# Kernel tuning notes

Measured on AMD Instinct MI355X. Metric: run time of the kernel, lower is better.

The kernel has to match this reference:

```python
import jax, jax.numpy as jnp
import numpy as np

EMBD_SIZE = 128
NUM_HEADS = 8
HEAD_SIZE = 16

def setup_inputs() -> dict:
    key = jax.random.key(0)
    ks = jax.random.split(key, 6)
    B, S = 8, 2048
    x = jax.random.normal(ks[0], (B, S, EMBD_SIZE), dtype=jnp.float32)
    # per-head Linear weights, torch layout [out, in] stacked over heads -> [H, hs, E]
    sc = 1.0 / np.sqrt(EMBD_SIZE)
    Wk = jax.random.normal(ks[1], (NUM_HEADS, HEAD_SIZE, EMBD_SIZE), dtype=jnp.float32) * sc
    Wq = jax.random.normal(ks[2], (NUM_HEADS, HEAD_SIZE, EMBD_SIZE), dtype=jnp.float32) * sc
    Wv = jax.random.normal(ks[3], (NUM_HEADS, HEAD_SIZE, EMBD_SIZE), dtype=jnp.float32) * sc
    Wp = jax.random.normal(ks[4], (EMBD_SIZE, NUM_HEADS * HEAD_SIZE), dtype=jnp.float32) * sc
    bp = jax.random.normal(ks[5], (EMBD_SIZE,), dtype=jnp.float32) * 0.01
    return {"x": x, "Wk": Wk, "Wq": Wq, "Wv": Wv, "Wp": Wp, "bp": bp}

def reference(x, Wk, Wq, Wv, Wp, bp):
    # x: [B,S,E]; W{k,q,v}: [H,hs,E]; Wp: [E,H*hs]
    B, S, E = x.shape
    H, hs, _ = Wk.shape
    q = jnp.einsum('bse,hde->bhsd', x, Wq)
    k = jnp.einsum('bse,hde->bhsd', x, Wk)
    v = jnp.einsum('bse,hde->bhsd', x, Wv)
    # NOTE: original code MULTIPLIES by sqrt(head_size) (k.shape[-1]**0.5)
    scores = jnp.einsum('bhsd,bhtd->bhst', q, k) * (hs ** 0.5)
    wei = jax.nn.softmax(scores, axis=-1)  # dropout is identity in eval mode
    out = jnp.einsum('bhst,bhtd->bhsd', wei, v)
    # concat heads along last dim: [B,S,H*hs]
    out = out.transpose(0, 2, 1, 3).reshape(B, S, H * hs)
    return out @ Wp.T + bp
```

## Files before the change

kernel.cpp:

```cpp
#include <hip/hip_runtime.h>
#include <hip/hip_bf16.h>

constexpr int Bb  = 8;
constexpr int Ss  = 2048;
constexpr int Ee  = 128;
constexpr int Hh  = 8;
constexpr int HSs = 16;
constexpr int QKVSZ = Bb * Hh * Ss * HSs;

typedef _Float16 f16;
typedef __attribute__((ext_vector_type(8)))  _Float16 f16x8;
typedef __attribute__((ext_vector_type(16))) float f32x16;

constexpr float QSCALE = 5.770780163555854f;

__device__ __forceinline__ unsigned pack_rtz(float lo, float hi) {
    union { __fp16 __attribute__((ext_vector_type(2))) h; unsigned u; } c;
    c.h = __builtin_amdgcn_cvt_pkrtz(lo, hi);
    return c.u;
}
__device__ __forceinline__ unsigned pack_rne(float lo, float hi) {
    union { __attribute__((ext_vector_type(2))) _Float16 h; unsigned u; } c;
    c.h[0] = (f16)lo; c.h[1] = (f16)hi;
    return c.u;
}

__global__ __launch_bounds__(256) void prep_kernel(
    const float* __restrict__ Wq, const float* __restrict__ Wk,
    const float* __restrict__ Wv, const float* __restrict__ Wp,
    f16* __restrict__ wh, f16* __restrict__ vo)
{
    const int idx = blockIdx.x * 256 + threadIdx.x;
    if (idx < 16384) {
        const int i = idx * 4;
        const float* src = (i < 16384) ? (Wq + i)
                         : (i < 32768) ? (Wk + i - 16384)
                         : (i < 49152) ? (Wv + i - 32768) : (Wp + i - 49152);
        float4 v = *(const float4*)src;
        union { f16 h[4]; uint2 u; } c;
        c.h[0] = (f16)v.x; c.h[1] = (f16)v.y; c.h[2] = (f16)v.z; c.h[3] = (f16)v.w;
        *(uint2*)(wh + i) = c.u;
    } else {
        const int p = idx - 16384;
        const int lane32 = p & 31, g = (p >> 5) & 3, it = (p >> 7) & 31, bh = p >> 12;
        const int lanep = 16 + (lane32 & 15) + (lane32 >> 4) * 32;
        const unsigned one2 = 0x3C003C00u;
        uint4 val = ((lane32 & 15) == 0) ? (uint4){one2, one2, one2, one2}
                                         : (uint4){0, 0, 0, 0};
        *(uint4*)(vo + (size_t)bh * 65536 + it * 2048 + g * 512 + lanep * 8) = val;
    }
}

__global__ __launch_bounds__(256) void qkv_kernel(
    const float* __restrict__ x, const f16* __restrict__ wh,
    f16* __restrict__ qo, f16* __restrict__ ko, f16* __restrict__ vo)
{
    constexpr int LDW = 136;
    __shared__ __align__(16) f16 Xs[32 * LDW];

    const int rowbase = blockIdx.x * 32;

    for (int idx = threadIdx.x; idx < 32 * 32; idx += 256) {
        const int r = idx >> 5, cp = idx & 31;
        float4 v = *(const float4*)(x + (size_t)(rowbase + r) * Ee + cp * 4);
        union { f16 h[4]; uint2 u; } c;
        c.h[0] = (f16)v.x; c.h[1] = (f16)v.y; c.h[2] = (f16)v.z; c.h[3] = (f16)v.w;
        *(uint2*)&Xs[r * LDW + cp * 4] = c.u;
    }
    __syncthreads();

    const int wv_ = threadIdx.x >> 6, lane = threadIdx.x & 63;
    const int h = lane >> 5, n31 = lane & 31;

    f16x8 A[8];
#pragma unroll
    for (int t = 0; t < 8; ++t)
        A[t] = *(const f16x8*)&Xs[n31 * LDW + 16 * t + 8 * h];
    __syncthreads();

    const int c = wv_ * 32 + n31;
    const int b = rowbase >> 11;
    const int s0 = rowbase & 2047;
    const int head = c >> 4, d = c & 15;
    const int bh = b * Hh + head;

    {
        const f16* wr = wh + 2 * 16384 + (size_t)c * Ee + 8 * h;
        f32x16 acc = {};
#pragma unroll
        for (int t = 0; t < 8; ++t)
            acc = __builtin_amdgcn_mfma_f32_32x32x16_f16(A[t], *(const f16x8*)(wr + 16 * t), acc, 0, 0, 0);
#pragma unroll
        for (int r = 0; r < 16; ++r) {
            const int row = (r & 3) + 8 * (r >> 2) + 4 * h;
            Xs[row * LDW + c] = (f16)acc[r];
        }
    }

#pragma unroll
    for (int mat = 0; mat < 2; ++mat) {
        const f16* wr = wh + mat * 16384 + (size_t)c * Ee + 8 * h;
        f32x16 acc = {};
#pragma unroll
        for (int t = 0; t < 8; ++t)
            acc = __builtin_amdgcn_mfma_f32_32x32x16_f16(A[t], *(const f16x8*)(wr + 16 * t), acc, 0, 0, 0);
        f16* dst = (mat == 0) ? qo : ko;
        const float scale = (mat == 1) ? QSCALE : 1.f;
#pragma unroll
        for (int r = 0; r < 16; ++r) {
            const int s = s0 + (r & 3) + 8 * (r >> 2) + 4 * h;
            dst[((size_t)bh * Ss + s) * HSs + d] = (f16)(acc[r] * scale);
        }
    }
    __syncthreads();

    const int it = s0 >> 6, g0 = (s0 >> 4) & 3;
    for (int p = threadIdx.x; p < 512; p += 256) {
        const int gl = p >> 8, hd = (p >> 5) & 7, dd = (p >> 1) & 15, eh = p & 1;
        union { f16 hv[8]; uint4 u; } pkt;
#pragma unroll
        for (int j = 0; j < 8; ++j)
            pkt.hv[j] = Xs[(gl * 16 + eh * 8 + j) * LDW + hd * 16 + dd];
        *(uint4*)(vo + (size_t)(b * Hh + hd) * 65536 + it * 2048
                  + (g0 + gl) * 512 + (dd + 32 * eh) * 8) = pkt.u;
    }
}

__device__ __forceinline__ void cb_exchange(const unsigned* pw, int h,
                                            f16x8& Blo, f16x8& Bhi) {
    unsigned exa = (unsigned)__shfl_xor((int)(h ? pw[0] : pw[2]), 32, 64);
    unsigned exb = (unsigned)__shfl_xor((int)(h ? pw[1] : pw[3]), 32, 64);
    unsigned exc = (unsigned)__shfl_xor((int)(h ? pw[4] : pw[6]), 32, 64);
    unsigned exd = (unsigned)__shfl_xor((int)(h ? pw[5] : pw[7]), 32, 64);
    union { unsigned u[4]; f16x8 v; } B1, B2;
    if (h == 0) {
        B1.u[0] = pw[0]; B1.u[1] = pw[1]; B1.u[2] = exa; B1.u[3] = exb;
        B2.u[0] = pw[4]; B2.u[1] = pw[5]; B2.u[2] = exc; B2.u[3] = exd;
    } else {
        B1.u[0] = exa; B1.u[1] = exb; B1.u[2] = pw[2]; B1.u[3] = pw[3];
        B2.u[0] = exc; B2.u[1] = exd; B2.u[2] = pw[6]; B2.u[3] = pw[7];
    }
    Blo = B1.v; Bhi = B2.v;
}

__global__ __launch_bounds__(128, 3) void attn_kernel(
    const f16* __restrict__ qg, const f16* __restrict__ kg,
    const f16* __restrict__ vg, f16* __restrict__ og)
{
    __shared__ float cmb[32 * 20];

    const int blk  = blockIdx.x;
    const int bh   = (blk & 7) * 8 + (blk >> 9);
    const int qblk = (blk >> 3) & 63;
    const int wv_  = threadIdx.x >> 6;
    const int lane = threadIdx.x & 63;
    const int h    = lane >> 5;
    const int q31  = lane & 31;
    const int qbase = qblk * 32;

    const f16x8 qf = *(const f16x8*)(qg + ((size_t)bh * Ss + qbase + q31) * HSs + 8 * h);

    const f16* pk = kg + (size_t)bh * Ss * HSs + wv_ * 1024 * HSs + q31 * 16 + 8 * h;
    const f16* pv = vg + (size_t)bh * 65536 + wv_ * 32768 + lane * 8;

    f16x8 ka0 = *(const f16x8*)pk;
    f16x8 ka1 = *(const f16x8*)(pk + 512);
    f16x8 va0 = *(const f16x8*)(pv);
    f16x8 va1 = *(const f16x8*)(pv + 512);
    f16x8 va2 = *(const f16x8*)(pv + 1024);
    f16x8 va3 = *(const f16x8*)(pv + 1536);

    f32x16 acc = {};
    const f32x16 z16 = {};
    float m = -1e30f;

    for (int it = 0; it < 16; ++it) {
        f16x8 nk0, nk1, nv0, nv1, nv2, nv3;
        if (it < 15) {
            pk += 1024; pv += 2048;
            nk0 = *(const f16x8*)pk;
            nk1 = *(const f16x8*)(pk + 512);
            nv0 = *(const f16x8*)(pv);
            nv1 = *(const f16x8*)(pv + 512);
            nv2 = *(const f16x8*)(pv + 1024);
            nv3 = *(const f16x8*)(pv + 1536);
        }

        f32x16 st0 = __builtin_amdgcn_mfma_f32_32x32x16_f16(ka0, qf, z16, 0, 0, 0);
        f32x16 st1 = __builtin_amdgcn_mfma_f32_32x32x16_f16(ka1, qf, z16, 0, 0, 0);

        float t0[8];
#pragma unroll
        for (int t = 0; t < 8; ++t)
            t0[t] = fmaxf(fmaxf(st0[t], st0[t + 8]), fmaxf(st1[t], st1[t + 8]));
#pragma unroll
        for (int t = 0; t < 4; ++t) t0[t] = fmaxf(t0[t], t0[t + 4]);
        float mx = fmaxf(fmaxf(t0[0], t0[1]), fmaxf(t0[2], t0[3]));
        mx = fmaxf(mx, __shfl_xor(mx, 32, 64));
        const float mnew = fmaxf(m, mx);
        const float corr = __builtin_amdgcn_exp2f(m - mnew);
#pragma unroll
        for (int r = 0; r < 9; ++r) acc[r] *= corr;
        m = mnew;

#pragma unroll
        for (int t = 0; t < 16; ++t) st0[t] = __builtin_amdgcn_exp2f(st0[t] - mnew);
#pragma unroll
        for (int t = 0; t < 16; ++t) st1[t] = __builtin_amdgcn_exp2f(st1[t] - mnew);
        unsigned pw0[8], pw1[8];
#pragma unroll
        for (int r = 0; r < 8; ++r) pw0[r] = pack_rtz(st0[2 * r], st0[2 * r + 1]);
#pragma unroll
        for (int r = 0; r < 8; ++r) pw1[r] = pack_rtz(st1[2 * r], st1[2 * r + 1]);
        f16x8 B1, B2, B3, B4;
        cb_exchange(pw0, h, B1, B2);
        cb_exchange(pw1, h, B3, B4);

        acc = __builtin_amdgcn_mfma_f32_32x32x16_f16(va0, B1, acc, 0, 0, 0);
        acc = __builtin_amdgcn_mfma_f32_32x32x16_f16(va1, B2, acc, 0, 0, 0);
        acc = __builtin_amdgcn_mfma_f32_32x32x16_f16(va2, B3, acc, 0, 0, 0);
        acc = __builtin_amdgcn_mfma_f32_32x32x16_f16(va3, B4, acc, 0, 0, 0);

        ka0 = nk0; ka1 = nk1;
        va0 = nv0; va1 = nv1; va2 = nv2; va3 = nv3;
    }

    const float lp = acc[8] + __shfl_xor(acc[8], 32, 64);

    if (wv_ == 1) {
        float* base = &cmb[q31 * 20];
#pragma unroll
        for (int j = 0; j < 4; ++j) { base[4 * h + j] = acc[j]; base[8 + 4 * h + j] = acc[4 + j]; }
        base[16] = lp; base[17] = m;
    }
    __syncthreads();
    if (wv_ == 0) {
        const float* base = &cmb[q31 * 20];
        const float l2 = base[16], m2 = base[17];
        const float M  = fmaxf(m, m2);
        const float c1 = __builtin_amdgcn_exp2f(m - M);
        const float c2 = __builtin_amdgcn_exp2f(m2 - M);
        const float l  = lp * c1 + l2 * c2;
        const float inv = 1.f / l;
        float o[8];
#pragma unroll
        for (int j = 0; j < 4; ++j) {
            o[j]     = (acc[j]     * c1 + base[4 * h + j]     * c2) * inv;
            o[4 + j] = (acc[4 + j] * c1 + base[8 + 4 * h + j] * c2) * inv;
        }
        const int b = bh >> 3, head = bh & 7;
        f16* op = og + ((size_t)b * Ss + qbase + q31) * Ee + head * HSs;
        uint2 lo = { pack_rne(o[0], o[1]), pack_rne(o[2], o[3]) };
        uint2 hi = { pack_rne(o[4], o[5]), pack_rne(o[6], o[7]) };
        *(uint2*)(op + 4 * h)     = lo;
        *(uint2*)(op + 8 + 4 * h) = hi;
    }
}

__global__ __launch_bounds__(256) void proj_kernel(
    const f16* __restrict__ oh, const f16* __restrict__ wph,
    const float* __restrict__ bp, float* __restrict__ out)
{
    constexpr int LDW = 136;
    __shared__ __align__(16) f16 Os[32 * LDW];
    const int rowbase = blockIdx.x * 32;

    for (int idx = threadIdx.x; idx < 512; idx += 256) {
        const int r = idx >> 4, cp = idx & 15;
        *(f16x8*)&Os[r * LDW + cp * 8] =
            *(const f16x8*)(oh + (size_t)(rowbase + r) * Ee + cp * 8);
    }
    __syncthreads();

    const int wv_ = threadIdx.x >> 6, lane = threadIdx.x & 63;
    const int h = lane >> 5, n31 = lane & 31;

    f16x8 A[8];
#pragma unroll
    for (int t = 0; t < 8; ++t)
        A[t] = *(const f16x8*)&Os[n31 * LDW + 16 * t + 8 * h];

    const int e = wv_ * 32 + n31;
    const f16* wr = wph + (size_t)e * Ee + 8 * h;
    f32x16 acc = {};
#pragma unroll
    for (int t = 0; t < 8; ++t)
        acc = __builtin_amdgcn_mfma_f32_32x32x16_f16(A[t], *(const f16x8*)(wr + 16 * t), acc, 0, 0, 0);

    const float bias = bp[e];
#pragma unroll
    for (int r = 0; r < 16; ++r) {
        const int R = rowbase + (r & 3) + 8 * (r >> 2) + 4 * h;
        out[(size_t)R * Ee + e] = acc[r] + bias;
    }
}

extern "C" void kernel_launch(void* const* d_in, const int* in_sizes, int n_in,
                              void* d_out, int out_size, void* d_ws, size_t ws_size,
                              hipStream_t stream)
{
    const float* x  = (const float*)d_in[0];
    const float* Wk = (const float*)d_in[1];
    const float* Wq = (const float*)d_in[2];
    const float* Wv = (const float*)d_in[3];
    const float* Wp = (const float*)d_in[4];
    const float* bp = (const float*)d_in[5];
    float* out = (float*)d_out;

    f16* ws = (f16*)d_ws;
    f16* qh = ws;
    f16* kh = ws + (size_t)QKVSZ;
    f16* vh = ws + (size_t)2 * QKVSZ;
    f16* oh = ws + (size_t)4 * QKVSZ;
    f16* wh = ws + (size_t)5 * QKVSZ;

    prep_kernel<<<1088, 256, 0, stream>>>(Wq, Wk, Wv, Wp, wh, vh);
    qkv_kernel<<<Bb * Ss / 32, 256, 0, stream>>>(x, wh, qh, kh, vh);
    attn_kernel<<<Bb * Hh * (Ss / 32), 128, 0, stream>>>(qh, kh, vh, oh);
    proj_kernel<<<Bb * Ss / 32, 256, 0, stream>>>(oh, wh + 49152, bp, out);
}
```

Before: 142.3 us.

## Fuse output projection into attention kernel, one wave per head

```diff
diff --git a/kernel.cpp b/kernel.cpp
--- a/kernel.cpp
+++ b/kernel.cpp
@@ -143,25 +143,28 @@
     Blo = B1.v; Bhi = B2.v;
 }
 
-__global__ __launch_bounds__(128, 3) void attn_kernel(
+__global__ __launch_bounds__(512, 2) void attn_kernel(
     const f16* __restrict__ qg, const f16* __restrict__ kg,
-    const f16* __restrict__ vg, f16* __restrict__ og)
-{
-    __shared__ float cmb[32 * 20];
+    const f16* __restrict__ vg, const f16* __restrict__ wph,
+    const float* __restrict__ bp, float* __restrict__ out)
+{
+    constexpr int LDW = 136;
+    __shared__ __align__(16) f16 Os[32 * LDW];
 
     const int blk  = blockIdx.x;
-    const int bh   = (blk & 7) * 8 + (blk >> 9);
-    const int qblk = (blk >> 3) & 63;
+    const int b    = blk & 7;
+    const int qblk = blk >> 3;
     const int wv_  = threadIdx.x >> 6;
     const int lane = threadIdx.x & 63;
     const int h    = lane >> 5;
     const int q31  = lane & 31;
     const int qbase = qblk * 32;
+    const int bh   = b * Hh + wv_;
 
     const f16x8 qf = *(const f16x8*)(qg + ((size_t)bh * Ss + qbase + q31) * HSs + 8 * h);
 
-    const f16* pk = kg + (size_t)bh * Ss * HSs + wv_ * 1024 * HSs + q31 * 16 + 8 * h;
-    const f16* pv = vg + (size_t)bh * 65536 + wv_ * 32768 + lane * 8;
+    const f16* pk = kg + (size_t)bh * Ss * HSs + q31 * 16 + 8 * h;
+    const f16* pv = vg + (size_t)bh * 65536 + lane * 8;
 
     f16x8 ka0 = *(const f16x8*)pk;
     f16x8 ka1 = *(const f16x8*)(pk + 512);
@@ -174,9 +177,9 @@
     const f32x16 z16 = {};
     float m = -1e30f;
 
-    for (int it = 0; it < 16; ++it) {
+    for (int it = 0; it < Ss / 64; ++it) {
         f16x8 nk0, nk1, nv0, nv1, nv2, nv3;
-        if (it < 15) {
+        if (it < Ss / 64 - 1) {
             pk += 1024; pv += 2048;
             nk0 = *(const f16x8*)pk;
             nk1 = *(const f16x8*)(pk + 512);
@@ -225,73 +228,38 @@
         va0 = nv0; va1 = nv1; va2 = nv2; va3 = nv3;
     }
 
-    const float lp = acc[8] + __shfl_xor(acc[8], 32, 64);
-
-    if (wv_ == 1) {
-        float* base = &cmb[q31 * 20];
-#pragma unroll
-        for (int j = 0; j < 4; ++j) { base[4 * h + j] = acc[j]; base[8 + 4 * h + j] = acc[4 + j]; }
-        base[16] = lp; base[17] = m;
-    }
-    __syncthreads();
-    if (wv_ == 0) {
-        const float* base = &cmb[q31 * 20];
-        const float l2 = base[16], m2 = base[17];
-        const float M  = fmaxf(m, m2);
-        const float c1 = __builtin_amdgcn_exp2f(m - M);
-        const float c2 = __builtin_amdgcn_exp2f(m2 - M);
-        const float l  = lp * c1 + l2 * c2;
-        const float inv = 1.f / l;
-        float o[8];
-#pragma unroll
-        for (int j = 0; j < 4; ++j) {
-            o[j]     = (acc[j]     * c1 + base[4 * h + j]     * c2) * inv;
-            o[4 + j] = (acc[4 + j] * c1 + base[8 + 4 * h + j] * c2) * inv;
-        }
-        const int b = bh >> 3, head = bh & 7;
-        f16* op = og + ((size_t)b * Ss + qbase + q31) * Ee + head * HSs;
-        uint2 lo = { pack_rne(o[0], o[1]), pack_rne(o[2], o[3]) };
-        uint2 hi = { pack_rne(o[4], o[5]), pack_rne(o[6], o[7]) };
-        *(uint2*)(op + 4 * h)     = lo;
-        *(uint2*)(op + 8 + 4 * h) = hi;
-    }
-}
-
-__global__ __launch_bounds__(256) void proj_kernel(
-    const f16* __restrict__ oh, const f16* __restrict__ wph,
-    const float* __restrict__ bp, float* __restrict__ out)
-{
-    constexpr int LDW = 136;
-    __shared__ __align__(16) f16 Os[32 * LDW];
-    const int rowbase = blockIdx.x * 32;
-
-    for (int idx = threadIdx.x; idx < 512; idx += 256) {
-        const int r = idx >> 4, cp = idx & 15;
-        *(f16x8*)&Os[r * LDW + cp * 8] =
-            *(const f16x8*)(oh + (size_t)(rowbase + r) * Ee + cp * 8);
-    }
-    __syncthreads();
-
-    const int wv_ = threadIdx.x >> 6, lane = threadIdx.x & 63;
-    const int h = lane >> 5, n31 = lane & 31;
-
-    f16x8 A[8];
-#pragma unroll
-    for (int t = 0; t < 8; ++t)
-        A[t] = *(const f16x8*)&Os[n31 * LDW + 16 * t + 8 * h];
-
-    const int e = wv_ * 32 + n31;
-    const f16* wr = wph + (size_t)e * Ee + 8 * h;
-    f32x16 acc = {};
-#pragma unroll
-    for (int t = 0; t < 8; ++t)
-        acc = __builtin_amdgcn_mfma_f32_32x32x16_f16(A[t], *(const f16x8*)(wr + 16 * t), acc, 0, 0, 0);
-
-    const float bias = bp[e];
-#pragma unroll
-    for (int r = 0; r < 16; ++r) {
-        const int R = rowbase + (r & 3) + 8 * (r >> 2) + 4 * h;
-        out[(size_t)R * Ee + e] = acc[r] + bias;
+    const float l = acc[8] + __shfl_xor(acc[8], 32, 64);
+    const float inv = 1.f / l;
+    {
+        unsigned w0 = pack_rne(acc[0] * inv, acc[1] * inv);
+        unsigned w1 = pack_rne(acc[2] * inv, acc[3] * inv);
+        unsigned w2 = pack_rne(acc[4] * inv, acc[5] * inv);
+        unsigned w3 = pack_rne(acc[6] * inv, acc[7] * inv);
+        f16* od = &Os[q31 * LDW + wv_ * HSs];
+        *(uint2*)(od + 4 * h)     = (uint2){w0, w1};
+        *(uint2*)(od + 8 + 4 * h) = (uint2){w2, w3};
+    }
+    __syncthreads();
+
+    if (wv_ < 4) {
+        f16x8 A[8];
+#pragma unroll
+        for (int t = 0; t < 8; ++t)
+            A[t] = *(const f16x8*)&Os[q31 * LDW + 16 * t + 8 * h];
+
+        const int e = wv_ * 32 + q31;
+        const f16* wr = wph + (size_t)e * Ee + 8 * h;
+        f32x16 pacc = {};
+#pragma unroll
+        for (int t = 0; t < 8; ++t)
+            pacc = __builtin_amdgcn_mfma_f32_32x32x16_f16(A[t], *(const f16x8*)(wr + 16 * t), pacc, 0, 0, 0);
+
+        const float bias = bp[e];
+#pragma unroll
+        for (int r = 0; r < 16; ++r) {
+            const int R = qbase + (r & 3) + 8 * (r >> 2) + 4 * h;
+            out[((size_t)b * Ss + R) * Ee + e] = pacc[r] + bias;
+        }
     }
 }
 
@@ -311,11 +279,9 @@
     f16* qh = ws;
     f16* kh = ws + (size_t)QKVSZ;
     f16* vh = ws + (size_t)2 * QKVSZ;
-    f16* oh = ws + (size_t)4 * QKVSZ;
-    f16* wh = ws + (size_t)5 * QKVSZ;
+    f16* wh = ws + (size_t)4 * QKVSZ;
 
     prep_kernel<<<1088, 256, 0, stream>>>(Wq, Wk, Wv, Wp, wh, vh);
     qkv_kernel<<<Bb * Ss / 32, 256, 0, stream>>>(x, wh, qh, kh, vh);
-    attn_kernel<<<Bb * Hh * (Ss / 32), 128, 0, stream>>>(qh, kh, vh, oh);
-    proj_kernel<<<Bb * Ss / 32, 256, 0, stream>>>(oh, wh + 49152, bp, out);
-}
+    attn_kernel<<<Bb * (Ss / 32), 512, 0, stream>>>(qh, kh, vh, wh + 49152, bp, out);
+}
```

Result: faster. 138.5 us (-2.7%).
